# Kernel optimization log

Hardware: AMD Instinct MI355X
Metric: run time of the kernel (lower is better)

## Reference

```python
import jax, jax.numpy as jnp
import numpy as np

DIM = 2048
N_HEADS = 32
N_KV_HEADS = 8
HEAD_DIM = DIM // N_HEADS  # 64
N_REP = N_HEADS // N_KV_HEADS  # 4
BSZ = 2
SEQ = 2048


def setup_inputs() -> dict:
    key = jax.random.key(0)
    ks = jax.random.split(key, 7)
    s = 0.02
    return {
        "x": jax.random.normal(ks[0], (BSZ, SEQ, DIM), dtype=jnp.float32),
        "freqs_cos": jnp.cos(jnp.outer(jnp.arange(SEQ, dtype=jnp.float32),
                                       1.0 / (10000.0 ** (jnp.arange(0, HEAD_DIM, 2, dtype=jnp.float32) / HEAD_DIM)))),
        "freqs_sin": jnp.sin(jnp.outer(jnp.arange(SEQ, dtype=jnp.float32),
                                       1.0 / (10000.0 ** (jnp.arange(0, HEAD_DIM, 2, dtype=jnp.float32) / HEAD_DIM)))),
        "wq": jax.random.normal(ks[1], (DIM, N_HEADS * HEAD_DIM), dtype=jnp.float32) * s,
        "wk": jax.random.normal(ks[2], (DIM, N_KV_HEADS * HEAD_DIM), dtype=jnp.float32) * s,
        "wv": jax.random.normal(ks[3], (DIM, N_KV_HEADS * HEAD_DIM), dtype=jnp.float32) * s,
        "wo": jax.random.normal(ks[4], (N_HEADS * HEAD_DIM, DIM), dtype=jnp.float32) * s,
    }


def _apply_rope(t, cos, sin):
    # t: [b, s, h, hd]; cos/sin: [s, hd/2] -> broadcast [1, s, 1, hd/2]
    tr = t.reshape(t.shape[:-1] + (HEAD_DIM // 2, 2))
    t_r, t_i = tr[..., 0], tr[..., 1]
    c = cos[None, :, None, :]
    s = sin[None, :, None, :]
    out_r = t_r * c - t_i * s
    out_i = t_r * s + t_i * c
    return jnp.stack([out_r, out_i], axis=-1).reshape(t.shape)


def reference(x, freqs_cos, freqs_sin, wq, wk, wv, wo):
    b, s, _ = x.shape
    xq = (x @ wq).reshape(b, s, N_HEADS, HEAD_DIM)
    xk = (x @ wk).reshape(b, s, N_KV_HEADS, HEAD_DIM)
    xv = (x @ wv).reshape(b, s, N_KV_HEADS, HEAD_DIM)

    xq = _apply_rope(xq, freqs_cos, freqs_sin)
    xk = _apply_rope(xk, freqs_cos, freqs_sin)

    # GQA: group query heads over kv heads instead of materializing repeated KV
    # xq -> [b, kv_heads, n_rep, s, hd]
    q = xq.transpose(0, 2, 1, 3).reshape(b, N_KV_HEADS, N_REP, s, HEAD_DIM)
    k = xk.transpose(0, 2, 1, 3)  # [b, kv, s, hd]
    v = xv.transpose(0, 2, 1, 3)  # [b, kv, s, hd]

    scale = 1.0 / jnp.sqrt(jnp.asarray(HEAD_DIM, dtype=x.dtype))
    scores = jnp.einsum("bgrqd,bgkd->bgrqk", q, k) * scale  # [b,kv,rep,s,s]
    causal = jnp.tril(jnp.ones((s, s), dtype=bool))
    scores = jnp.where(causal[None, None, None], scores, jnp.finfo(scores.dtype).min)
    probs = jax.nn.softmax(scores, axis=-1)
    out = jnp.einsum("bgrqk,bgkd->bgrqd", probs, v)  # [b,kv,rep,s,hd]
    out = out.reshape(b, N_HEADS, s, HEAD_DIM).transpose(0, 2, 1, 3).reshape(b, s, N_HEADS * HEAD_DIM)
    return out @ wo
```

## Files before the change

kernel.cpp:

```cpp
#include <hip/hip_runtime.h>

typedef unsigned short u16;
typedef unsigned int u32;
typedef __bf16 bf16x4 __attribute__((ext_vector_type(4)));
typedef __bf16 bf16x8 __attribute__((ext_vector_type(8)));
typedef float f32x4 __attribute__((ext_vector_type(4)));
typedef u32 u32x4 __attribute__((ext_vector_type(4)));

struct __align__(4) U16x2 { u16 x, y; };
struct __align__(8) U16x4 { u16 x, y, z, w; };

#define DEV static __device__ __forceinline__

extern "C" __device__ float __ocml_exp2_f32(float);
#if __has_builtin(__builtin_amdgcn_exp2f)
#define EXP2(x) __builtin_amdgcn_exp2f(x)
#else
#define EXP2(x) __ocml_exp2_f32(x)
#endif

DEV u16 f2bf(float f) {
  __bf16 h = (__bf16)f;
  return __builtin_bit_cast(u16, h);
}
DEV u32 pk2bf(float lo, float hi) { return (u32)f2bf(lo) | ((u32)f2bf(hi) << 16); }

DEV void gload16(const void* g, void* l) {
  __builtin_amdgcn_global_load_lds((const __attribute__((address_space(1))) char*)g,
                                   (__attribute__((address_space(3))) char*)l, 16, 0, 0);
}

DEV f32x4 mfma16(bf16x8 a, bf16x8 b, f32x4 c) {
  return __builtin_amdgcn_mfma_f32_16x16x32_bf16(a, b, c, 0, 0, 0);
}

__global__ __launch_bounds__(256) void cvt_x(const float* __restrict__ x, u16* __restrict__ xb) {
  int i = blockIdx.x * 256 + threadIdx.x;
  float4 v = ((const float4*)x)[i];
  U16x4 o;
  o.x = f2bf(v.x); o.y = f2bf(v.y); o.z = f2bf(v.z); o.w = f2bf(v.w);
  ((U16x4*)xb)[i] = o;
}

__global__ __launch_bounds__(256) void tconv(const float* __restrict__ src, u16* __restrict__ dst,
                                             int C, int nOff, int ldd) {
  __shared__ float t[32][33];
  int bx = blockIdx.x, by = blockIdx.y;
  int tx = threadIdx.x, ty = threadIdx.y;
#pragma unroll
  for (int j = 0; j < 4; ++j)
    t[ty + 8 * j][tx] = src[(size_t)(by * 32 + ty + 8 * j) * C + bx * 32 + tx];
  __syncthreads();
#pragma unroll
  for (int j = 0; j < 4; ++j)
    dst[(size_t)(nOff + bx * 32 + ty + 8 * j) * ldd + by * 32 + tx] = f2bf(t[tx][ty + 8 * j]);
}

__global__ __launch_bounds__(256) void vtrans(const u16* __restrict__ Vsl, u16* __restrict__ Vt) {
  __shared__ u16 t[32][33];
  int bx = blockIdx.x, by = blockIdx.y, bz = blockIdx.z;
  int tx = threadIdx.x, ty = threadIdx.y;
  int b = bz >> 3, kh = bz & 7;
  const u16* src = Vsl + (size_t)(b * 2048 + bx * 32) * 512 + kh * 64 + by * 32;
#pragma unroll
  for (int j = 0; j < 4; ++j) t[ty + 8 * j][tx] = src[(size_t)(ty + 8 * j) * 512 + tx];
  __syncthreads();
  u16* dst = Vt + ((size_t)bz * 64 + by * 32) * 2048 + bx * 32;
#pragma unroll
  for (int j = 0; j < 4; ++j) dst[(size_t)(ty + 8 * j) * 2048 + tx] = t[tx][ty + 8 * j];
}

__global__ __launch_bounds__(256, 2) void gemm_qkv(const u16* __restrict__ A,
                                                   const u16* __restrict__ BT,
                                                   const float* __restrict__ fc,
                                                   const float* __restrict__ fs,
                                                   u16* __restrict__ Qo,
                                                   u16* __restrict__ Ko,
                                                   u16* __restrict__ Vsl) {
  __shared__ __align__(16) char smem[65536];
  const int tid = threadIdx.x;
  const int lane = tid & 63;
  const int wm = (tid >> 7) & 1, wn = (tid >> 6) & 1;
  const int tm = blockIdx.y, tn = blockIdx.x;
  const int K = 2048, Kb = 4096;

  f32x4 acc[4][4];
#pragma unroll
  for (int i = 0; i < 4; ++i)
#pragma unroll
    for (int j = 0; j < 4; ++j) acc[i][j] = (f32x4){0.f, 0.f, 0.f, 0.f};

  const char* Ag = (const char*)A + (size_t)tm * 128 * Kb;
  const char* Bg = (const char*)BT + (size_t)tn * 128 * Kb;

  auto stage = [&](int buf, int t) {
#pragma unroll
    for (int i = 0; i < 4; ++i) {
      int vt = i * 256 + tid;
      int row = vt >> 3;
      int cb = (((vt & 7) << 4) ^ ((row & 7) << 4));
      gload16(Ag + (size_t)row * Kb + t * 128 + cb, smem + buf * 16384 + vt * 16);
      gload16(Bg + (size_t)row * Kb + t * 128 + cb, smem + 32768 + buf * 16384 + vt * 16);
    }
  };

  stage(0, 0);
  int cur = 0;
  const int NT = K >> 6;
  for (int t = 0; t < NT; ++t) {
    __syncthreads();
    if (t + 1 < NT) stage(cur ^ 1, t + 1);
    const char* As = smem + cur * 16384;
    const char* Bs = smem + 32768 + cur * 16384;
#pragma unroll
    for (int ks = 0; ks < 2; ++ks) {
      bf16x8 a[4], b[4];
#pragma unroll
      for (int mf = 0; mf < 4; ++mf) {
        int row = wm * 64 + mf * 16 + (lane & 15);
        int cb = (ks * 64 + ((lane >> 4) << 4)) ^ ((row & 7) << 4);
        a[mf] = *(const bf16x8*)(As + row * 128 + cb);
      }
#pragma unroll
      for (int nf = 0; nf < 4; ++nf) {
        int row = wn * 64 + nf * 16 + (lane & 15);
        int cb = (ks * 64 + ((lane >> 4) << 4)) ^ ((row & 7) << 4);
        b[nf] = *(const bf16x8*)(Bs + row * 128 + cb);
      }
#pragma unroll
      for (int mf = 0; mf < 4; ++mf)
#pragma unroll
        for (int nf = 0; nf < 4; ++nf) acc[mf][nf] = mfma16(a[mf], b[nf], acc[mf][nf]);
    }
    cur ^= 1;
  }

  const float QS = 0.18033688011112042f;
#pragma unroll
  for (int mf = 0; mf < 4; ++mf) {
    int row0 = tm * 128 + wm * 64 + mf * 16 + ((lane >> 4) << 2);
#pragma unroll
    for (int nf = 0; nf < 4; ++nf) {
      int col = tn * 128 + wn * 64 + nf * 16 + (lane & 15);
      if (col < 2560) {
        int d = col & 63, d2 = d >> 1;
        bool ev = !(col & 1);
        bool isQ = (col < 2048);
        int hh = isQ ? (col >> 6) : ((col - 2048) >> 6);
#pragma unroll
        for (int r = 0; r < 4; ++r) {
          int row = row0 + r;
          int bb = row >> 11, s = row & 2047;
          float v = acc[mf][nf][r];
          float p = __shfl_xor(v, 1, 64);
          float c = fc[s * 32 + d2], sn = fs[s * 32 + d2];
          if (isQ) { c *= QS; sn *= QS; }
          float o = ev ? (v * c - p * sn) : (v * c + p * sn);
          if (isQ)
            Qo[((size_t)(bb * 32 + hh) * 2048 + s) * 64 + d] = f2bf(o);
          else
            Ko[((size_t)(bb * 8 + hh) * 2048 + s) * 64 + d] = f2bf(o);
        }
      } else {
#pragma unroll
        for (int r = 0; r < 4; ++r)
          Vsl[(size_t)(row0 + r) * 512 + (col - 2560)] = f2bf(acc[mf][nf][r]);
      }
    }
  }
}

__global__ __launch_bounds__(256, 2) void gemm_bt(const u16* __restrict__ A,
                                                  const u16* __restrict__ BT,
                                                  float* __restrict__ C,
                                                  int M, int N, int K) {
  __shared__ __align__(16) char smem[65536];
  const int tid = threadIdx.x;
  const int lane = tid & 63;
  const int wm = (tid >> 7) & 1, wn = (tid >> 6) & 1;
  const int tm = blockIdx.y, tn = blockIdx.x;
  const int Kb = K * 2;

  f32x4 acc[4][4];
#pragma unroll
  for (int i = 0; i < 4; ++i)
#pragma unroll
    for (int j = 0; j < 4; ++j) acc[i][j] = (f32x4){0.f, 0.f, 0.f, 0.f};

  const char* Ag = (const char*)A + (size_t)tm * 128 * Kb;
  const char* Bg = (const char*)BT + (size_t)tn * 128 * Kb;

  auto stage = [&](int buf, int t) {
#pragma unroll
    for (int i = 0; i < 4; ++i) {
      int vt = i * 256 + tid;
      int row = vt >> 3;
      int cb = (((vt & 7) << 4) ^ ((row & 7) << 4));
      gload16(Ag + (size_t)row * Kb + t * 128 + cb, smem + buf * 16384 + vt * 16);
      gload16(Bg + (size_t)row * Kb + t * 128 + cb, smem + 32768 + buf * 16384 + vt * 16);
    }
  };

  stage(0, 0);
  int cur = 0;
  const int NT = K >> 6;
  for (int t = 0; t < NT; ++t) {
    __syncthreads();
    if (t + 1 < NT) stage(cur ^ 1, t + 1);
    const char* As = smem + cur * 16384;
    const char* Bs = smem + 32768 + cur * 16384;
#pragma unroll
    for (int ks = 0; ks < 2; ++ks) {
      bf16x8 a[4], b[4];
#pragma unroll
      for (int mf = 0; mf < 4; ++mf) {
        int row = wm * 64 + mf * 16 + (lane & 15);
        int cb = (ks * 64 + ((lane >> 4) << 4)) ^ ((row & 7) << 4);
        a[mf] = *(const bf16x8*)(As + row * 128 + cb);
      }
#pragma unroll
      for (int nf = 0; nf < 4; ++nf) {
        int row = wn * 64 + nf * 16 + (lane & 15);
        int cb = (ks * 64 + ((lane >> 4) << 4)) ^ ((row & 7) << 4);
        b[nf] = *(const bf16x8*)(Bs + row * 128 + cb);
      }
#pragma unroll
      for (int mf = 0; mf < 4; ++mf)
#pragma unroll
        for (int nf = 0; nf < 4; ++nf) acc[mf][nf] = mfma16(a[mf], b[nf], acc[mf][nf]);
    }
    cur ^= 1;
  }
#pragma unroll
  for (int mf = 0; mf < 4; ++mf) {
    int row0 = tm * 128 + wm * 64 + mf * 16 + ((lane >> 4) << 2);
#pragma unroll
    for (int nf = 0; nf < 4; ++nf) {
      int col = tn * 128 + wn * 64 + nf * 16 + (lane & 15);
#pragma unroll
      for (int r = 0; r < 4; ++r)
        C[(size_t)(row0 + r) * N + col] = acc[mf][nf][r];
    }
  }
}

__global__ __launch_bounds__(128, 4) void attn(const u16* __restrict__ Q,
                                               const u16* __restrict__ Kt,
                                               const u16* __restrict__ Vt,
                                               u16* __restrict__ O) {
  __shared__ __align__(16) char smem[16384];

  const int tid = threadIdx.x, lane = tid & 63, w = tid >> 6;
  const int q15 = lane & 15, g = lane >> 4;
  const int bx = blockIdx.x, h = blockIdx.y, b = blockIdx.z;
  const int kh = h >> 2;
  const int QT0 = 63 - bx, QT1 = bx;

  const char* Qg = (const char*)(Q + ((size_t)(b * 32 + h) * 2048) * 64);
  const char* Kg = (const char*)(Kt + ((size_t)(b * 8 + kh) * 2048 * 64));
  const char* Vg = (const char*)(Vt + ((size_t)(b * 8 + kh) * 64 * 2048));

  bf16x8 qf0[2], qf1[2];
#pragma unroll
  for (int ks = 0; ks < 2; ++ks) {
    int r0 = QT0 * 32 + w * 16 + q15;
    int r1 = QT1 * 32 + w * 16 + q15;
    qf0[ks] = *(const bf16x8*)(Qg + (size_t)r0 * 128 + ks * 64 + (g << 4));
    qf1[ks] = *(const bf16x8*)(Qg + (size_t)r1 * 128 + ks * 64 + (g << 4));
  }

  f32x4 acc0[4], acc1[4];
#pragma unroll
  for (int j = 0; j < 4; ++j) {
    acc0[j] = (f32x4){0.f, 0.f, 0.f, 0.f};
    acc1[j] = (f32x4){0.f, 0.f, 0.f, 0.f};
  }
  float m0 = -1e30f, m1 = -1e30f, l0 = 0.f, l1 = 0.f;
  const f32x4 FZ = (f32x4){0.f, 0.f, 0.f, 0.f};

  auto stageKV = [&](int buf, int kt) {
#pragma unroll
    for (int i = 0; i < 2; ++i) {
      int vt = i * 128 + tid;
      int rho = vt >> 3, ck = vt & 7;
      int kap = ((rho & 12) << 1) + ((rho & 16) >> 2) + (rho & 3);
      gload16(Kg + (size_t)(kt * 32 + kap) * 128 + (((ck ^ rho) & 7) << 4),
              smem + buf * 8192 + vt * 16);
      int d = vt >> 2, cv = vt & 3;
      gload16(Vg + (size_t)d * 4096 + kt * 64 + (((cv ^ (d >> 1)) & 3) << 4),
              smem + buf * 8192 + 4096 + vt * 16);
    }
  };

  stageKV(0, 0);
  int cur = 0;
  const int nkt = QT0 + 1;
  for (int kt = 0; kt < nkt; ++kt) {
    __syncthreads();
    if (kt + 1 < nkt) stageKV(cur ^ 1, kt + 1);
    const char* Ks = smem + cur * 8192;
    const char* Vs = smem + cur * 8192 + 4096;
    const bool la = (kt <= QT1);

    bf16x8 kf[2][2];
#pragma unroll
    for (int ks = 0; ks < 2; ++ks)
#pragma unroll
      for (int nf = 0; nf < 2; ++nf) {
        int r = nf * 16 + q15;
        int c = (4 * ks + g) ^ (r & 7);
        kf[ks][nf] = *(const bf16x8*)(Ks + r * 128 + (c << 4));
      }

    f32x4 st0[2], st1[2];
    __builtin_amdgcn_s_setprio(1);
#pragma unroll
    for (int nf = 0; nf < 2; ++nf) {
      st0[nf] = mfma16(kf[0][nf], qf0[0], FZ);
      st0[nf] = mfma16(kf[1][nf], qf0[1], st0[nf]);
    }
    if (la) {
#pragma unroll
      for (int nf = 0; nf < 2; ++nf) {
        st1[nf] = mfma16(kf[0][nf], qf1[0], FZ);
        st1[nf] = mfma16(kf[1][nf], qf1[1], st1[nf]);
      }
    }
    __builtin_amdgcn_s_setprio(0);

    if (kt == QT0) {
      int qg = QT0 * 32 + w * 16 + q15;
#pragma unroll
      for (int nf = 0; nf < 2; ++nf)
#pragma unroll
        for (int r = 0; r < 4; ++r) {
          int kg = kt * 32 + 8 * g + 4 * nf + r;
          if (kg > qg) st0[nf][r] = -1e30f;
        }
    }
    if (la && kt == QT1) {
      int qg = QT1 * 32 + w * 16 + q15;
#pragma unroll
      for (int nf = 0; nf < 2; ++nf)
#pragma unroll
        for (int r = 0; r < 4; ++r) {
          int kg = kt * 32 + 8 * g + 4 * nf + r;
          if (kg > qg) st1[nf][r] = -1e30f;
        }
    }

    bf16x8 pa0, pa1;
#pragma unroll
    for (int t = 0; t < 2; ++t) {
      if (t == 1 && !la) break;
      f32x4* st = (t == 0) ? st0 : st1;
      float& m_r = (t == 0) ? m0 : m1;
      float& l_r = (t == 0) ? l0 : l1;
      f32x4* accT = (t == 0) ? acc0 : acc1;

      float vm = fmaxf(fmaxf(fmaxf(st[0][0], st[0][1]), fmaxf(st[0][2], st[0][3])),
                       fmaxf(fmaxf(st[1][0], st[1][1]), fmaxf(st[1][2], st[1][3])));
      if (!__all(vm - m_r <= 8.0f)) {
        vm = fmaxf(vm, __shfl_xor(vm, 16, 64));
        vm = fmaxf(vm, __shfl_xor(vm, 32, 64));
        float mn = fmaxf(m_r, vm);
        float cr = EXP2(m_r - mn);
        m_r = mn;
        l_r *= cr;
        float cra[4];
#pragma unroll
        for (int r = 0; r < 4; ++r) cra[r] = __shfl(cr, 4 * g + r, 64);
#pragma unroll
        for (int nfd = 0; nfd < 4; ++nfd)
#pragma unroll
          for (int r = 0; r < 4; ++r) accT[nfd][r] *= cra[r];
      }
      float p0 = EXP2(st[0][0] - m_r), p1 = EXP2(st[0][1] - m_r);
      float p2 = EXP2(st[0][2] - m_r), p3 = EXP2(st[0][3] - m_r);
      float p4 = EXP2(st[1][0] - m_r), p5 = EXP2(st[1][1] - m_r);
      float p6 = EXP2(st[1][2] - m_r), p7 = EXP2(st[1][3] - m_r);
      l_r += ((p0 + p1) + (p2 + p3)) + ((p4 + p5) + (p6 + p7));
      u32x4 W;
      W.x = pk2bf(p0, p1);
      W.y = pk2bf(p2, p3);
      W.z = pk2bf(p4, p5);
      W.w = pk2bf(p6, p7);
      if (t == 0) pa0 = __builtin_bit_cast(bf16x8, W);
      else pa1 = __builtin_bit_cast(bf16x8, W);
    }

#pragma unroll
    for (int nfd = 0; nfd < 4; ++nfd) {
      int d = nfd * 16 + q15;
      int c = (g ^ (d >> 1)) & 3;
      bf16x8 vb = *(const bf16x8*)(Vs + d * 64 + (c << 4));
      __builtin_amdgcn_s_setprio(1);
      acc0[nfd] = mfma16(pa0, vb, acc0[nfd]);
      if (la) acc1[nfd] = mfma16(pa1, vb, acc1[nfd]);
      __builtin_amdgcn_s_setprio(0);
    }
    cur ^= 1;
  }

#pragma unroll
  for (int t = 0; t < 2; ++t) {
    float l_r = (t == 0) ? l0 : l1;
    l_r += __shfl_xor(l_r, 16, 64);
    l_r += __shfl_xor(l_r, 32, 64);
    f32x4* accT = (t == 0) ? acc0 : acc1;
    int qt = (t == 0) ? QT0 : QT1;
    u16* Og = O + ((size_t)(b * 2048 + qt * 32 + w * 16) * 2048 + h * 64);
    float la4[4];
#pragma unroll
    for (int r = 0; r < 4; ++r) la4[r] = __shfl(l_r, 4 * g + r, 64);
#pragma unroll
    for (int r = 0; r < 4; ++r) {
      float li = 1.f / la4[r];
#pragma unroll
      for (int nfd = 0; nfd < 4; ++nfd)
        Og[(size_t)(4 * g + r) * 2048 + nfd * 16 + q15] = f2bf(accT[nfd][r] * li);
    }
  }
}

extern "C" void kernel_launch(void* const* d_in, const int* in_sizes, int n_in,
                              void* d_out, int out_size, void* d_ws, size_t ws_size,
                              hipStream_t stream) {
  const float* x = (const float*)d_in[0];
  const float* fc = (const float*)d_in[1];
  const float* fs = (const float*)d_in[2];
  const float* wq = (const float*)d_in[3];
  const float* wk = (const float*)d_in[4];
  const float* wv = (const float*)d_in[5];
  const float* wo = (const float*)d_in[6];
  float* out = (float*)d_out;
  char* ws = (char*)d_ws;

  u16* xb    = (u16*)(ws);
  u16* Qb    = (u16*)(ws + 16777216);
  u16* Kb    = (u16*)(ws + 33554432);
  u16* Vsl   = (u16*)(ws + 37748736);
  u16* Vtb   = (u16*)(ws + 41943040);
  u16* woT   = (u16*)(ws + 46137344);
  u16* wqkvT = (u16*)(ws + 54525952);
  u16* Obuf = xb;

  dim3 tb(32, 8);
  cvt_x<<<dim3(8192), dim3(256), 0, stream>>>(x, xb);
  tconv<<<dim3(64, 64), tb, 0, stream>>>(wq, wqkvT, 2048, 0, 2048);
  tconv<<<dim3(16, 64), tb, 0, stream>>>(wk, wqkvT, 512, 2048, 2048);
  tconv<<<dim3(16, 64), tb, 0, stream>>>(wv, wqkvT, 512, 2560, 2048);
  tconv<<<dim3(64, 64), tb, 0, stream>>>(wo, woT, 2048, 0, 2048);
  gemm_qkv<<<dim3(24, 32), dim3(256), 0, stream>>>(xb, wqkvT, fc, fs, Qb, Kb, Vsl);
  vtrans<<<dim3(64, 2, 16), tb, 0, stream>>>(Vsl, Vtb);
  attn<<<dim3(32, 32, 2), dim3(128), 0, stream>>>(Qb, Kb, Vtb, Obuf);
  gemm_bt<<<dim3(16, 32), dim3(256), 0, stream>>>(Obuf, woT, out, 4096, 2048, 2048);
}
```

Measured before the change: 203.8 us.

## Merge prep kernels into one launch and compute softmax row sums via MFMA

The x conversion and four weight transpose-convert kernels are merged into a single launch that dispatches on block index, cutting four launches and their tail gaps. Separately, the attention kernel no longer accumulates the softmax denominator with scalar adds and cross-lane shuffles; it runs an extra MFMA of the bf16 probabilities against a ones vector, which yields per-row sums already laid out like the output accumulator. The row max now folds in the running max directly. Side effects: the denominator is summed from bf16-rounded probabilities, which matches the numerator, and each tile adds one or two MFMAs.

```diff
diff --git a/kernel.cpp b/kernel.cpp
--- a/kernel.cpp
+++ b/kernel.cpp
@@ -34,26 +34,41 @@
   return __builtin_amdgcn_mfma_f32_16x16x32_bf16(a, b, c, 0, 0, 0);
 }
 
-__global__ __launch_bounds__(256) void cvt_x(const float* __restrict__ x, u16* __restrict__ xb) {
-  int i = blockIdx.x * 256 + threadIdx.x;
-  float4 v = ((const float4*)x)[i];
-  U16x4 o;
-  o.x = f2bf(v.x); o.y = f2bf(v.y); o.z = f2bf(v.z); o.w = f2bf(v.w);
-  ((U16x4*)xb)[i] = o;
-}
-
-__global__ __launch_bounds__(256) void tconv(const float* __restrict__ src, u16* __restrict__ dst,
-                                             int C, int nOff, int ldd) {
+__global__ __launch_bounds__(256) void prep(const float* __restrict__ x,
+                                            const float* __restrict__ wq,
+                                            const float* __restrict__ wk,
+                                            const float* __restrict__ wv,
+                                            const float* __restrict__ wo,
+                                            u16* __restrict__ xb,
+                                            u16* __restrict__ wqkvT,
+                                            u16* __restrict__ woT) {
   __shared__ float t[32][33];
-  int bx = blockIdx.x, by = blockIdx.y;
+  int id = blockIdx.x;
   int tx = threadIdx.x, ty = threadIdx.y;
+  if (id < 8192) {
+    int i = id * 256 + ty * 32 + tx;
+    float4 v = ((const float4*)x)[i];
+    U16x4 o;
+    o.x = f2bf(v.x); o.y = f2bf(v.y); o.z = f2bf(v.z); o.w = f2bf(v.w);
+    ((U16x4*)xb)[i] = o;
+    return;
+  }
+  id -= 8192;
+  const float* src;
+  u16* dst;
+  int C, nOff, gx;
+  if (id < 4096)      { src = wq; dst = wqkvT; C = 2048; nOff = 0;    gx = 64; }
+  else if (id < 5120) { id -= 4096; src = wk; dst = wqkvT; C = 512; nOff = 2048; gx = 16; }
+  else if (id < 6144) { id -= 5120; src = wv; dst = wqkvT; C = 512; nOff = 2560; gx = 16; }
+  else                { id -= 6144; src = wo; dst = woT;   C = 2048; nOff = 0;   gx = 64; }
+  int bx = id % gx, by = id / gx;
 #pragma unroll
   for (int j = 0; j < 4; ++j)
     t[ty + 8 * j][tx] = src[(size_t)(by * 32 + ty + 8 * j) * C + bx * 32 + tx];
   __syncthreads();
 #pragma unroll
   for (int j = 0; j < 4; ++j)
-    dst[(size_t)(nOff + bx * 32 + ty + 8 * j) * ldd + by * 32 + tx] = f2bf(t[tx][ty + 8 * j]);
+    dst[(size_t)(nOff + bx * 32 + ty + 8 * j) * 2048 + by * 32 + tx] = f2bf(t[tx][ty + 8 * j]);
 }
 
 __global__ __launch_bounds__(256) void vtrans(const u16* __restrict__ Vsl, u16* __restrict__ Vt) {
@@ -260,6 +275,10 @@
   const char* Kg = (const char*)(Kt + ((size_t)(b * 8 + kh) * 2048 * 64));
   const char* Vg = (const char*)(Vt + ((size_t)(b * 8 + kh) * 64 * 2048));
 
+  u32x4 onesW;
+  onesW.x = onesW.y = onesW.z = onesW.w = 0x3F803F80u;
+  const bf16x8 ONES = __builtin_bit_cast(bf16x8, onesW);
+
   bf16x8 qf0[2], qf1[2];
 #pragma unroll
   for (int ks = 0; ks < 2; ++ks) {
@@ -269,13 +288,15 @@
     qf1[ks] = *(const bf16x8*)(Qg + (size_t)r1 * 128 + ks * 64 + (g << 4));
   }
 
-  f32x4 acc0[4], acc1[4];
+  f32x4 acc0[4], acc1[4], accl0, accl1;
 #pragma unroll
   for (int j = 0; j < 4; ++j) {
     acc0[j] = (f32x4){0.f, 0.f, 0.f, 0.f};
     acc1[j] = (f32x4){0.f, 0.f, 0.f, 0.f};
   }
-  float m0 = -1e30f, m1 = -1e30f, l0 = 0.f, l1 = 0.f;
+  accl0 = (f32x4){0.f, 0.f, 0.f, 0.f};
+  accl1 = (f32x4){0.f, 0.f, 0.f, 0.f};
+  float m0 = -1e30f, m1 = -1e30f;
   const f32x4 FZ = (f32x4){0.f, 0.f, 0.f, 0.f};
 
   auto stageKV = [&](int buf, int kt) {
@@ -355,18 +376,17 @@
       if (t == 1 && !la) break;
       f32x4* st = (t == 0) ? st0 : st1;
       float& m_r = (t == 0) ? m0 : m1;
-      float& l_r = (t == 0) ? l0 : l1;
       f32x4* accT = (t == 0) ? acc0 : acc1;
-
-      float vm = fmaxf(fmaxf(fmaxf(st[0][0], st[0][1]), fmaxf(st[0][2], st[0][3])),
-                       fmaxf(fmaxf(st[1][0], st[1][1]), fmaxf(st[1][2], st[1][3])));
+      f32x4& acclT = (t == 0) ? accl0 : accl1;
+
+      float vm = fmaxf(fmaxf(fmaxf(fmaxf(st[0][0], st[0][1]), st[0][2]),
+                             fmaxf(fmaxf(st[0][3], st[1][0]), st[1][1])),
+                       fmaxf(fmaxf(st[1][2], st[1][3]), m_r));
       if (!__all(vm - m_r <= 8.0f)) {
         vm = fmaxf(vm, __shfl_xor(vm, 16, 64));
         vm = fmaxf(vm, __shfl_xor(vm, 32, 64));
-        float mn = fmaxf(m_r, vm);
-        float cr = EXP2(m_r - mn);
-        m_r = mn;
-        l_r *= cr;
+        float cr = EXP2(m_r - vm);
+        m_r = vm;
         float cra[4];
 #pragma unroll
         for (int r = 0; r < 4; ++r) cra[r] = __shfl(cr, 4 * g + r, 64);
@@ -374,17 +394,14 @@
         for (int nfd = 0; nfd < 4; ++nfd)
 #pragma unroll
           for (int r = 0; r < 4; ++r) accT[nfd][r] *= cra[r];
-      }
-      float p0 = EXP2(st[0][0] - m_r), p1 = EXP2(st[0][1] - m_r);
-      float p2 = EXP2(st[0][2] - m_r), p3 = EXP2(st[0][3] - m_r);
-      float p4 = EXP2(st[1][0] - m_r), p5 = EXP2(st[1][1] - m_r);
-      float p6 = EXP2(st[1][2] - m_r), p7 = EXP2(st[1][3] - m_r);
-      l_r += ((p0 + p1) + (p2 + p3)) + ((p4 + p5) + (p6 + p7));
+#pragma unroll
+        for (int r = 0; r < 4; ++r) acclT[r] *= cra[r];
+      }
       u32x4 W;
-      W.x = pk2bf(p0, p1);
-      W.y = pk2bf(p2, p3);
-      W.z = pk2bf(p4, p5);
-      W.w = pk2bf(p6, p7);
+      W.x = pk2bf(EXP2(st[0][0] - m_r), EXP2(st[0][1] - m_r));
+      W.y = pk2bf(EXP2(st[0][2] - m_r), EXP2(st[0][3] - m_r));
+      W.z = pk2bf(EXP2(st[1][0] - m_r), EXP2(st[1][1] - m_r));
+      W.w = pk2bf(EXP2(st[1][2] - m_r), EXP2(st[1][3] - m_r));
       if (t == 0) pa0 = __builtin_bit_cast(bf16x8, W);
       else pa1 = __builtin_bit_cast(bf16x8, W);
     }
@@ -399,23 +416,22 @@
       if (la) acc1[nfd] = mfma16(pa1, vb, acc1[nfd]);
       __builtin_amdgcn_s_setprio(0);
     }
+    __builtin_amdgcn_s_setprio(1);
+    accl0 = mfma16(pa0, ONES, accl0);
+    if (la) accl1 = mfma16(pa1, ONES, accl1);
+    __builtin_amdgcn_s_setprio(0);
     cur ^= 1;
   }
 
 #pragma unroll
   for (int t = 0; t < 2; ++t) {
-    float l_r = (t == 0) ? l0 : l1;
-    l_r += __shfl_xor(l_r, 16, 64);
-    l_r += __shfl_xor(l_r, 32, 64);
     f32x4* accT = (t == 0) ? acc0 : acc1;
+    f32x4 acclT = (t == 0) ? accl0 : accl1;
     int qt = (t == 0) ? QT0 : QT1;
     u16* Og = O + ((size_t)(b * 2048 + qt * 32 + w * 16) * 2048 + h * 64);
-    float la4[4];
-#pragma unroll
-    for (int r = 0; r < 4; ++r) la4[r] = __shfl(l_r, 4 * g + r, 64);
 #pragma unroll
     for (int r = 0; r < 4; ++r) {
-      float li = 1.f / la4[r];
+      float li = 1.f / acclT[r];
 #pragma unroll
       for (int nfd = 0; nfd < 4; ++nfd)
         Og[(size_t)(4 * g + r) * 2048 + nfd * 16 + q15] = f2bf(accT[nfd][r] * li);
@@ -446,11 +462,7 @@
   u16* Obuf = xb;
 
   dim3 tb(32, 8);
-  cvt_x<<<dim3(8192), dim3(256), 0, stream>>>(x, xb);
-  tconv<<<dim3(64, 64), tb, 0, stream>>>(wq, wqkvT, 2048, 0, 2048);
-  tconv<<<dim3(16, 64), tb, 0, stream>>>(wk, wqkvT, 512, 2048, 2048);
-  tconv<<<dim3(16, 64), tb, 0, stream>>>(wv, wqkvT, 512, 2560, 2048);
-  tconv<<<dim3(64, 64), tb, 0, stream>>>(wo, woT, 2048, 0, 2048);
+  prep<<<dim3(18432), tb, 0, stream>>>(x, wq, wk, wv, wo, xb, wqkvT, woT);
   gemm_qkv<<<dim3(24, 32), dim3(256), 0, stream>>>(xb, wqkvT, fc, fs, Qb, Kb, Vsl);
   vtrans<<<dim3(64, 2, 16), tb, 0, stream>>>(Vsl, Vtb);
   attn<<<dim3(32, 32, 2), dim3(128), 0, stream>>>(Qb, Kb, Vtb, Obuf);
```

New measurement: 194.5 us. 4.6% less time.
